# Performance work log

Measured on AMD Instinct MI355X. Metric: run time of the kernel, lower is better.

Reference implementation:

```python
import jax, jax.numpy as jnp
import numpy as np

DIM = 1024
B, S = 4, 2048

def setup_inputs() -> dict:
    key = jax.random.key(0)
    ks = jax.random.split(key, 4)
    x = jax.random.normal(ks[0], (B, S, DIM), dtype=jnp.float32)
    mask = jax.random.randint(ks[1], (B, S, S), 0, 2, dtype=jnp.int32)
    Wqkv = jax.random.normal(ks[2], (DIM, 3 * DIM), dtype=jnp.float32) / np.sqrt(DIM)
    bqkv = jnp.zeros((3 * DIM,), dtype=jnp.float32)
    Wout = jax.random.normal(ks[3], (DIM, DIM), dtype=jnp.float32) / np.sqrt(DIM)
    bout = jnp.zeros((DIM,), dtype=jnp.float32)
    return {"x": x, "mask": mask, "Wqkv": Wqkv, "bqkv": bqkv, "Wout": Wout, "bout": bout}

def reference(x, mask, Wqkv, bqkv, Wout, bout):
    dim = x.shape[-1]
    qkv = x @ Wqkv + bqkv                      # [B,S,3*dim]
    q, k, v = jnp.split(qkv, 3, axis=-1)       # each [B,S,dim]
    scores = jnp.einsum('bqd,bkd->bqk', q, k) / jnp.sqrt(jnp.float32(dim))
    # faithful to torch: masked positions set to 1e-10 (NOT -inf)
    scores = jnp.where(mask == 0, jnp.float32(1e-10), scores)
    attn = jax.nn.softmax(scores, axis=-1)     # dropout is identity in eval
    out = jnp.einsum('bqk,bkd->bqd', attn, v)  # [B,S,dim]
    return out @ Wout + bout
```

## Files before the change

### kernel.cpp

```cpp
#include <hip/hip_runtime.h>


typedef __attribute__((ext_vector_type(8))) short short8;
typedef __attribute__((ext_vector_type(4))) float f32x4;
typedef unsigned short u16;

#define SEQ 2048
#define NB 4

static __device__ __forceinline__ u16 f2bf(float f) {
    unsigned int u = __builtin_bit_cast(unsigned int, f);
    u += 0x7fffu + ((u >> 16) & 1u);
    return (u16)(u >> 16);
}
static __device__ __forceinline__ float bf2f(u16 h) {
    unsigned int u = ((unsigned int)h) << 16;
    return __builtin_bit_cast(float, u);
}

static __device__ __forceinline__ void gld16(const u16* l, const u16* g) {
    __builtin_amdgcn_global_load_lds(
        (__attribute__((address_space(1))) void*)(g),
        (__attribute__((address_space(3))) void*)(l),
        16, 0, 0);
}

__global__ __launch_bounds__(256) void cvt_bf16(const float* __restrict__ s,
                                                u16* __restrict__ d, long n) {
    long i = ((long)blockIdx.x * 256 + threadIdx.x) * 8;
    if (i >= n) return;
    f32x4 a = *(const f32x4*)(s + i);
    f32x4 b = *(const f32x4*)(s + i + 4);
    short8 o;
    o[0] = (short)f2bf(a.x); o[1] = (short)f2bf(a.y);
    o[2] = (short)f2bf(a.z); o[3] = (short)f2bf(a.w);
    o[4] = (short)f2bf(b.x); o[5] = (short)f2bf(b.y);
    o[6] = (short)f2bf(b.z); o[7] = (short)f2bf(b.w);
    *(short8*)(d + i) = o;
}

__global__ __launch_bounds__(256) void transpose_cvt(const float* __restrict__ in,
                                                     u16* __restrict__ out,
                                                     int R, int C) {
    __shared__ float t[32][33];
    const int c0 = blockIdx.x * 32;
    const int r0 = blockIdx.y * 32;
    const int x = threadIdx.x & 31;
    const int y = (threadIdx.x >> 5) * 4;
    #pragma unroll
    for (int i = 0; i < 4; i++)
        t[y + i][x] = in[(long)(r0 + y + i) * C + c0 + x];
    __syncthreads();
    #pragma unroll
    for (int i = 0; i < 4; i++)
        out[(long)(c0 + y + i) * R + r0 + x] = f2bf(t[x][y + i]);
}

__global__ __launch_bounds__(256) void transpose_v(const u16* __restrict__ qkv,
                                                   u16* __restrict__ vt) {
    __shared__ u16 t[32][33];
    const int b = blockIdx.z;
    const int s0 = blockIdx.y * 32;
    const int d0 = blockIdx.x * 32;
    const int x = threadIdx.x & 31;
    const int y = (threadIdx.x >> 5) * 4;
    const u16* src = qkv + (long)b * SEQ * 3072 + 2048;
    u16* dst = vt + (long)b * 1024 * SEQ;
    #pragma unroll
    for (int i = 0; i < 4; i++)
        t[y + i][x] = src[(long)(s0 + y + i) * 3072 + d0 + x];
    __syncthreads();
    #pragma unroll
    for (int i = 0; i < 4; i++)
        dst[(long)(d0 + y + i) * SEQ + s0 + x] = t[x][y + i];
}

template<int EPI>
__global__ __launch_bounds__(512) void gemm256d(
    const u16* __restrict__ Ap, long lda, long aBatch,
    const u16* __restrict__ Bp, long ldb, long bBatch,
    void* __restrict__ Cp, long ldc, long cBatch,
    const float* __restrict__ bias, float scale, int K, int nbx)
{
    __shared__ __attribute__((aligned(16))) u16 lds[2][4][8192];

    const int T = K >> 6;
    const int tid = threadIdx.x;
    const int lane = tid & 63;
    const int wave = tid >> 6;
    const int wm = wave >> 2;
    const int wn = wave & 3;
    const int m16 = lane & 15;
    const int quad = lane >> 4;
    const int b = blockIdx.z;

    const int nwg = gridDim.x;
    int wg = blockIdx.x;
    if ((nwg & 7) == 0)
        wg = (wg & 7) * (nwg >> 3) + (wg >> 3);
    const int bx = wg % nbx;
    const int by = wg / nbx;
    const long gm0 = (long)by * 256;
    const long gn0 = (long)bx * 256;

    const u16* A = Ap + (long)b * aBatch;
    const u16* B = Bp + (long)b * bBatch;

    const int rl = lane >> 3;
    const int lsl = ((lane & 7) ^ rl) * 8;
    const long aR = gm0 + wave * 8 + rl;
    const long bR = gn0 + (wave >> 2) * 64 + (wave & 3) * 8 + rl;

#define STGD(sl, tt) do { \
    const long kc_ = (long)(tt) << 6; \
    u16* l_ = &lds[sl][0][0]; \
    gld16(l_ + 0 * 8192 + wave * 512,       A + (aR)       * lda + kc_ + lsl); \
    gld16(l_ + 0 * 8192 + (8 + wave) * 512, A + (aR + 128) * lda + kc_ + lsl); \
    gld16(l_ + 1 * 8192 + wave * 512,       A + (aR + 64)  * lda + kc_ + lsl); \
    gld16(l_ + 1 * 8192 + (8 + wave) * 512, A + (aR + 192) * lda + kc_ + lsl); \
    gld16(l_ + 2 * 8192 + wave * 512,       B + (bR)       * ldb + kc_ + lsl); \
    gld16(l_ + 2 * 8192 + (8 + wave) * 512, B + (bR + 128) * ldb + kc_ + lsl); \
    gld16(l_ + 3 * 8192 + wave * 512,       B + (bR + 32)  * ldb + kc_ + lsl); \
    gld16(l_ + 3 * 8192 + (8 + wave) * 512, B + (bR + 160) * ldb + kc_ + lsl); \
} while (0)

    const int s0 = quad ^ (m16 & 7);
    const int aBase = (wm * 64 + m16) * 64;
    const int bBase = (wn * 32 + m16) * 64;
    const int aoff0 = aBase + s0 * 8, aoff1 = aBase + (s0 ^ 4) * 8;
    const int boff0 = bBase + s0 * 8, boff1 = bBase + (s0 ^ 4) * 8;

    short8 aF[4][2], b0F[2][2], b1F[2][2];
    f32x4 acc[8][4];
    #pragma unroll
    for (int mi = 0; mi < 8; mi++)
        #pragma unroll
        for (int ni = 0; ni < 4; ni++)
            acc[mi][ni] = (f32x4){0.f, 0.f, 0.f, 0.f};

#define TILE_COMPUTE(sl) do { \
    const u16* l = &lds[sl][0][0]; \
    _Pragma("unroll") \
    for (int mfl = 0; mfl < 4; ++mfl) { \
        aF[mfl][0] = *(const short8*)(l + aoff0 + mfl * 1024); \
        aF[mfl][1] = *(const short8*)(l + aoff1 + mfl * 1024); \
    } \
    _Pragma("unroll") \
    for (int nj = 0; nj < 2; ++nj) { \
        b0F[nj][0] = *(const short8*)(l + 2 * 8192 + boff0 + nj * 1024); \
        b0F[nj][1] = *(const short8*)(l + 2 * 8192 + boff1 + nj * 1024); \
        b1F[nj][0] = *(const short8*)(l + 3 * 8192 + boff0 + nj * 1024); \
        b1F[nj][1] = *(const short8*)(l + 3 * 8192 + boff1 + nj * 1024); \
    } \
    _Pragma("unroll") \
    for (int mi = 0; mi < 4; ++mi) \
        _Pragma("unroll") \
        for (int nj = 0; nj < 4; ++nj) { \
            const short8* bf = (nj < 2) ? &b0F[nj][0] : &b1F[nj - 2][0]; \
            acc[mi][nj] = __builtin_amdgcn_mfma_f32_16x16x32_bf16( \
                aF[mi][0], bf[0], acc[mi][nj], 0, 0, 0); \
            acc[mi][nj] = __builtin_amdgcn_mfma_f32_16x16x32_bf16( \
                aF[mi][1], bf[1], acc[mi][nj], 0, 0, 0); \
        } \
    _Pragma("unroll") \
    for (int mfl = 0; mfl < 4; ++mfl) { \
        aF[mfl][0] = *(const short8*)(l + 1 * 8192 + aoff0 + mfl * 1024); \
        aF[mfl][1] = *(const short8*)(l + 1 * 8192 + aoff1 + mfl * 1024); \
    } \
    _Pragma("unroll") \
    for (int mi = 0; mi < 4; ++mi) \
        _Pragma("unroll") \
        for (int nj = 0; nj < 4; ++nj) { \
            const short8* bf = (nj < 2) ? &b0F[nj][0] : &b1F[nj - 2][0]; \
            acc[4 + mi][nj] = __builtin_amdgcn_mfma_f32_16x16x32_bf16( \
                aF[mi][0], bf[0], acc[4 + mi][nj], 0, 0, 0); \
            acc[4 + mi][nj] = __builtin_amdgcn_mfma_f32_16x16x32_bf16( \
                aF[mi][1], bf[1], acc[4 + mi][nj], 0, 0, 0); \
        } \
} while (0)

    STGD(0, 0);
    __syncthreads();

    for (int t = 0; t < T; t += 2) {
        if (t + 1 < T) STGD(1, t + 1);
        TILE_COMPUTE(0);
        __syncthreads();
        if (t + 2 < T) STGD(0, t + 2);
        TILE_COMPUTE(1);
        __syncthreads();
    }

    const long row0 = gm0 + wm * 128 + quad * 4;
    const long colbase = gn0 + wn * 64 + m16;
    if (EPI == 0 || EPI == 1) {
        u16* C = (u16*)Cp + (long)b * cBatch;
        float bv[4];
        #pragma unroll
        for (int ni = 0; ni < 4; ++ni)
            bv[ni] = (EPI == 0 && bias)
                   ? bias[colbase + (ni >> 1) * 32 + (ni & 1) * 16] : 0.f;
        #pragma unroll
        for (int mi = 0; mi < 8; ++mi) {
            const long rb = row0 + (mi >> 2) * 64 + (mi & 3) * 16;
            #pragma unroll
            for (int r = 0; r < 4; ++r) {
                u16* Crow = C + (rb + r) * ldc + colbase;
                #pragma unroll
                for (int ni = 0; ni < 4; ++ni) {
                    const float vv = (EPI == 1) ? acc[mi][ni][r] * scale
                                                : acc[mi][ni][r] + bv[ni];
                    Crow[(ni >> 1) * 32 + (ni & 1) * 16] = f2bf(vv);
                }
            }
        }
    } else {
        float* C = (float*)Cp + (long)b * cBatch;
        float bv[4];
        #pragma unroll
        for (int ni = 0; ni < 4; ++ni)
            bv[ni] = bias ? bias[colbase + (ni >> 1) * 32 + (ni & 1) * 16] : 0.f;
        #pragma unroll
        for (int mi = 0; mi < 8; ++mi) {
            const long rb = row0 + (mi >> 2) * 64 + (mi & 3) * 16;
            #pragma unroll
            for (int r = 0; r < 4; ++r) {
                float* Crow = C + (rb + r) * ldc + colbase;
                #pragma unroll
                for (int ni = 0; ni < 4; ++ni)
                    Crow[(ni >> 1) * 32 + (ni & 1) * 16] = acc[mi][ni][r] + bv[ni];
            }
        }
    }
#undef STGD
#undef TILE_COMPUTE
}

template<int EPI>
__global__ __launch_bounds__(512) void gemm192(
    const u16* __restrict__ Ap, long lda, long aBatch,
    const u16* __restrict__ Bp, long ldb, long bBatch,
    void* __restrict__ Cp, long ldc, long cBatch,
    const float* __restrict__ bias, float scale, int K, int nbx)
{
    __shared__ __attribute__((aligned(16))) u16 lds[2][28672];

    const int T = K >> 6;
    const int tid = threadIdx.x;
    const int lane = tid & 63;
    const int wave = tid >> 6;
    const int wm = wave >> 2;
    const int wn = wave & 3;
    const int m16 = lane & 15;
    const int quad = lane >> 4;
    const int b = blockIdx.z;

    const int nwg = gridDim.x;
    int wg = blockIdx.x;
    if ((nwg & 7) == 0)
        wg = (wg & 7) * (nwg >> 3) + (wg >> 3);
    const int bx = wg % nbx;
    const int by = wg / nbx;
    const long gm0 = (long)by * 256;
    const long gn0 = (long)bx * 192;

    const u16* A = Ap + (long)b * aBatch;
    const u16* B = Bp + (long)b * bBatch;

    const int rl = lane >> 3;
    const int lsl = ((lane & 7) ^ rl) * 8;
    const long aR = gm0 + wave * 8 + rl;
    const long bR = gn0 + wave * 8 + rl;

#define STG192(sl, tt) do { \
    const long kc_ = (long)(tt) << 6; \
    u16* l_ = &lds[sl][0]; \
    gld16(l_ + wave * 512,              A + (aR)       * lda + kc_ + lsl); \
    gld16(l_ + (8 + wave) * 512,        A + (aR + 128) * lda + kc_ + lsl); \
    gld16(l_ + 8192 + wave * 512,       A + (aR + 64)  * lda + kc_ + lsl); \
    gld16(l_ + 8192 + (8 + wave) * 512, A + (aR + 192) * lda + kc_ + lsl); \
    gld16(l_ + 16384 + wave * 512,        B + (bR)       * ldb + kc_ + lsl); \
    gld16(l_ + 16384 + (8 + wave) * 512,  B + (bR + 64)  * ldb + kc_ + lsl); \
    gld16(l_ + 16384 + (16 + wave) * 512, B + (bR + 128) * ldb + kc_ + lsl); \
} while (0)

    const int s0 = quad ^ (m16 & 7);
    const int aBase = (wm * 64 + m16) * 64;
    const int bBase = (wn * 48 + m16) * 64;
    const int aoff0 = aBase + s0 * 8, aoff1 = aBase + (s0 ^ 4) * 8;
    const int boff0 = bBase + s0 * 8, boff1 = bBase + (s0 ^ 4) * 8;

    short8 aF[4][2], bF[3][2];
    f32x4 acc[8][3];
    #pragma unroll
    for (int mi = 0; mi < 8; mi++)
        #pragma unroll
        for (int ni = 0; ni < 3; ni++)
            acc[mi][ni] = (f32x4){0.f, 0.f, 0.f, 0.f};

#define TILE192(sl) do { \
    const u16* l = &lds[sl][0]; \
    _Pragma("unroll") \
    for (int mfl = 0; mfl < 4; ++mfl) { \
        aF[mfl][0] = *(const short8*)(l + aoff0 + mfl * 1024); \
        aF[mfl][1] = *(const short8*)(l + aoff1 + mfl * 1024); \
    } \
    _Pragma("unroll") \
    for (int nj = 0; nj < 3; ++nj) { \
        bF[nj][0] = *(const short8*)(l + 16384 + boff0 + nj * 1024); \
        bF[nj][1] = *(const short8*)(l + 16384 + boff1 + nj * 1024); \
    } \
    _Pragma("unroll") \
    for (int mi = 0; mi < 4; ++mi) \
        _Pragma("unroll") \
        for (int nj = 0; nj < 3; ++nj) { \
            acc[mi][nj] = __builtin_amdgcn_mfma_f32_16x16x32_bf16( \
                aF[mi][0], bF[nj][0], acc[mi][nj], 0, 0, 0); \
            acc[mi][nj] = __builtin_amdgcn_mfma_f32_16x16x32_bf16( \
                aF[mi][1], bF[nj][1], acc[mi][nj], 0, 0, 0); \
        } \
    _Pragma("unroll") \
    for (int mfl = 0; mfl < 4; ++mfl) { \
        aF[mfl][0] = *(const short8*)(l + 8192 + aoff0 + mfl * 1024); \
        aF[mfl][1] = *(const short8*)(l + 8192 + aoff1 + mfl * 1024); \
    } \
    _Pragma("unroll") \
    for (int mi = 0; mi < 4; ++mi) \
        _Pragma("unroll") \
        for (int nj = 0; nj < 3; ++nj) { \
            acc[4 + mi][nj] = __builtin_amdgcn_mfma_f32_16x16x32_bf16( \
                aF[mi][0], bF[nj][0], acc[4 + mi][nj], 0, 0, 0); \
            acc[4 + mi][nj] = __builtin_amdgcn_mfma_f32_16x16x32_bf16( \
                aF[mi][1], bF[nj][1], acc[4 + mi][nj], 0, 0, 0); \
        } \
} while (0)

    STG192(0, 0);
    __syncthreads();

    for (int t = 0; t < T; t += 2) {
        if (t + 1 < T) STG192(1, t + 1);
        TILE192(0);
        __syncthreads();
        if (t + 2 < T) STG192(0, t + 2);
        TILE192(1);
        __syncthreads();
    }

    const long row0 = gm0 + wm * 128 + quad * 4;
    const long colbase = gn0 + wn * 48 + m16;
    if (EPI == 0 || EPI == 1) {
        u16* C = (u16*)Cp + (long)b * cBatch;
        float bv[3];
        #pragma unroll
        for (int ni = 0; ni < 3; ++ni)
            bv[ni] = (EPI == 0 && bias) ? bias[colbase + ni * 16] : 0.f;
        #pragma unroll
        for (int mi = 0; mi < 8; ++mi) {
            const long rb = row0 + (mi >> 2) * 64 + (mi & 3) * 16;
            #pragma unroll
            for (int r = 0; r < 4; ++r) {
                u16* Crow = C + (rb + r) * ldc + colbase;
                #pragma unroll
                for (int ni = 0; ni < 3; ++ni) {
                    const float vv = (EPI == 1) ? acc[mi][ni][r] * scale
                                                : acc[mi][ni][r] + bv[ni];
                    Crow[ni * 16] = f2bf(vv);
                }
            }
        }
    } else {
        float* C = (float*)Cp + (long)b * cBatch;
        float bv[3];
        #pragma unroll
        for (int ni = 0; ni < 3; ++ni)
            bv[ni] = bias ? bias[colbase + ni * 16] : 0.f;
        #pragma unroll
        for (int mi = 0; mi < 8; ++mi) {
            const long rb = row0 + (mi >> 2) * 64 + (mi & 3) * 16;
            #pragma unroll
            for (int r = 0; r < 4; ++r) {
                float* Crow = C + (rb + r) * ldc + colbase;
                #pragma unroll
                for (int ni = 0; ni < 3; ++ni)
                    Crow[ni * 16] = acc[mi][ni][r] + bv[ni];
            }
        }
    }
#undef STG192
#undef TILE192
}

template<int EPI>
__global__ __launch_bounds__(256, 2) void gemm128d(
    const u16* __restrict__ Ap, long lda, long aBatch,
    const u16* __restrict__ Bp, long ldb, long bBatch,
    void* __restrict__ Cp, long ldc, long cBatch,
    const float* __restrict__ bias, float scale, int K, int nbx)
{
    __shared__ __attribute__((aligned(16))) u16 lds[2][2][8192];

    const int T = K >> 6;
    const int tid = threadIdx.x;
    const int lane = tid & 63;
    const int wave = tid >> 6;
    const int wm = wave >> 1;
    const int wn = wave & 1;
    const int m16 = lane & 15;
    const int quad = lane >> 4;
    const int b = blockIdx.z;

    const int nwg = gridDim.x;
    int wg = blockIdx.x;
    if ((nwg & 7) == 0)
        wg = (wg & 7) * (nwg >> 3) + (wg >> 3);
    const int bx = wg % nbx;
    const int by = wg / nbx;
    const long m0 = (long)by * 128;
    const long n0 = (long)bx * 128;

    const u16* A = Ap + (long)b * aBatch;
    const u16* B = Bp + (long)b * bBatch;

    const int rl = lane >> 3;
    const int lsl = ((lane & 7) ^ rl) * 8;
    const long aR = m0 + wave * 8 + rl;
    const long bR = n0 + wave * 8 + rl;

#define STG128(sl, tt) do { \
    const long kc_ = (long)(tt) << 6; \
    _Pragma("unroll") \
    for (int i_ = 0; i_ < 4; ++i_) { \
        gld16(&lds[sl][0][(i_ * 4 + wave) * 512], A + (aR + i_ * 32) * lda + kc_ + lsl); \
        gld16(&lds[sl][1][(i_ * 4 + wave) * 512], B + (bR + i_ * 32) * ldb + kc_ + lsl); \
    } \
} while (0)

    const int s0 = quad ^ (m16 & 7);
    const int aoff0 = (wm * 64 + m16) * 64 + s0 * 8;
    const int aoff1 = (wm * 64 + m16) * 64 + (s0 ^ 4) * 8;
    const int boff0 = (wn * 64 + m16) * 64 + s0 * 8;
    const int boff1 = (wn * 64 + m16) * 64 + (s0 ^ 4) * 8;

    short8 aF[4][2], bF[4][2];
    f32x4 acc[4][4];
    #pragma unroll
    for (int mi = 0; mi < 4; mi++)
        #pragma unroll
        for (int ni = 0; ni < 4; ni++)
            acc[mi][ni] = (f32x4){0.f, 0.f, 0.f, 0.f};

#define TILE128(sl) do { \
    const u16* la = &lds[sl][0][0]; \
    const u16* lb = &lds[sl][1][0]; \
    _Pragma("unroll") \
    for (int mf = 0; mf < 4; ++mf) { \
        aF[mf][0] = *(const short8*)(la + aoff0 + mf * 1024); \
        aF[mf][1] = *(const short8*)(la + aoff1 + mf * 1024); \
    } \
    _Pragma("unroll") \
    for (int nj = 0; nj < 4; ++nj) { \
        bF[nj][0] = *(const short8*)(lb + boff0 + nj * 1024); \
        bF[nj][1] = *(const short8*)(lb + boff1 + nj * 1024); \
    } \
    _Pragma("unroll") \
    for (int mi = 0; mi < 4; ++mi) \
        _Pragma("unroll") \
        for (int nj = 0; nj < 4; ++nj) { \
            acc[mi][nj] = __builtin_amdgcn_mfma_f32_16x16x32_bf16( \
                aF[mi][0], bF[nj][0], acc[mi][nj], 0, 0, 0); \
            acc[mi][nj] = __builtin_amdgcn_mfma_f32_16x16x32_bf16( \
                aF[mi][1], bF[nj][1], acc[mi][nj], 0, 0, 0); \
        } \
} while (0)

    STG128(0, 0);
    __syncthreads();

    for (int t = 0; t < T; t += 2) {
        if (t + 1 < T) STG128(1, t + 1);
        TILE128(0);
        __syncthreads();
        if (t + 2 < T) STG128(0, t + 2);
        TILE128(1);
        __syncthreads();
    }

    const long row0 = m0 + wm * 64 + quad * 4;
    const long colbase = n0 + wn * 64 + m16;
    if (EPI == 0 || EPI == 1) {
        u16* C = (u16*)Cp + (long)b * cBatch;
        float bv[4];
        #pragma unroll
        for (int ni = 0; ni < 4; ++ni)
            bv[ni] = (EPI == 0 && bias) ? bias[colbase + ni * 16] : 0.f;
        #pragma unroll
        for (int mi = 0; mi < 4; ++mi)
            #pragma unroll
            for (int r = 0; r < 4; ++r) {
                u16* Crow = C + (row0 + mi * 16 + r) * ldc + colbase;
                #pragma unroll
                for (int ni = 0; ni < 4; ++ni) {
                    const float vv = (EPI == 1) ? acc[mi][ni][r] * scale
                                                : acc[mi][ni][r] + bv[ni];
                    Crow[ni * 16] = f2bf(vv);
                }
            }
    } else {
        float* C = (float*)Cp + (long)b * cBatch;
        float bv[4];
        #pragma unroll
        for (int ni = 0; ni < 4; ++ni)
            bv[ni] = bias ? bias[colbase + ni * 16] : 0.f;
        #pragma unroll
        for (int mi = 0; mi < 4; ++mi)
            #pragma unroll
            for (int r = 0; r < 4; ++r) {
                float* Crow = C + (row0 + mi * 16 + r) * ldc + colbase;
                #pragma unroll
                for (int ni = 0; ni < 4; ++ni)
                    Crow[ni * 16] = acc[mi][ni][r] + bv[ni];
            }
    }
#undef STG128
#undef TILE128
}

__global__ __launch_bounds__(256) void softmax2048(u16* __restrict__ S,
                                                   const int* __restrict__ mask) {
    const long row = blockIdx.x;
    u16* p = S + row * SEQ;
    const int* mrow = mask + row * SEQ;
    const int tid = threadIdx.x;

    short8 v = *(const short8*)(p + tid * 8);
    uint4 mw0 = *(const uint4*)(mrow + tid * 8);
    uint4 mw1 = *(const uint4*)(mrow + tid * 8 + 4);
    const unsigned int* mwv = (const unsigned int*)&mw0;

    float f[8];
    #pragma unroll
    for (int j = 0; j < 8; j++) {
        const unsigned int mv = (j < 4) ? mwv[j] : ((const unsigned int*)&mw1)[j - 4];
        f[j] = (mv == 0u) ? 1e-10f : bf2f((u16)v[j]);
    }

    float m = f[0];
    #pragma unroll
    for (int j = 1; j < 8; j++) m = fmaxf(m, f[j]);
    #pragma unroll
    for (int i = 1; i < 64; i <<= 1) m = fmaxf(m, __shfl_xor(m, i));

    __shared__ float redm[4], reds[4];
    if ((tid & 63) == 0) redm[tid >> 6] = m;
    __syncthreads();
    m = fmaxf(fmaxf(redm[0], redm[1]), fmaxf(redm[2], redm[3]));

    float e[8], s = 0.f;
    #pragma unroll
    for (int j = 0; j < 8; j++) { e[j] = __expf(f[j] - m); s += e[j]; }
    #pragma unroll
    for (int i = 1; i < 64; i <<= 1) s += __shfl_xor(s, i);
    if ((tid & 63) == 0) reds[tid >> 6] = s;
    __syncthreads();
    s = reds[0] + reds[1] + reds[2] + reds[3];

    const float inv = 1.f / s;
    short8 o;
    #pragma unroll
    for (int j = 0; j < 8; j++) o[j] = (short)f2bf(e[j] * inv);
    *(short8*)(p + tid * 8) = o;
}

extern "C" void kernel_launch(void* const* d_in, const int* in_sizes, int n_in,
                              void* d_out, int out_size, void* d_ws, size_t ws_size,
                              hipStream_t stream) {
    const float* x    = (const float*)d_in[0];
    const int*   mask = (const int*)d_in[1];
    const float* Wqkv = (const float*)d_in[2];
    const float* bqkv = (const float*)d_in[3];
    const float* Wout = (const float*)d_in[4];
    const float* bout = (const float*)d_in[5];
    float* out = (float*)d_out;

    char* ws = (char*)d_ws;
    u16* xh   = (u16*)(ws + 0);
    u16* wqt  = (u16*)(ws + 16777216);
    u16* sc   = (u16*)(ws + 0);
    u16* wot  = (u16*)(ws + 33554432);
    u16* qkv  = (u16*)(ws + 35651584);
    u16* attn = (u16*)(ws + 35651584);
    u16* vt   = (u16*)(ws + 85983232);

    cvt_bf16<<<4096, 256, 0, stream>>>(x, xh, 8388608);
    transpose_cvt<<<dim3(96, 32), 256, 0, stream>>>(Wqkv, wqt, 1024, 3072);
    transpose_cvt<<<dim3(32, 32), 256, 0, stream>>>(Wout, wot, 1024, 1024);

    gemm192<0><<<dim3(512, 1, 1), 512, 0, stream>>>(
        xh, 1024, 0, wqt, 1024, 0, qkv, 3072, 0, bqkv, 1.f, 1024, 16);

    transpose_v<<<dim3(32, 64, NB), 256, 0, stream>>>(qkv, vt);

    gemm256d<1><<<dim3(64, 1, NB), 512, 0, stream>>>(
        qkv, 3072, (long)SEQ * 3072, qkv + 1024, 3072, (long)SEQ * 3072,
        sc, SEQ, (long)SEQ * SEQ, nullptr, 0.03125f, 1024, 8);

    softmax2048<<<dim3(NB * SEQ), 256, 0, stream>>>(sc, mask);

    gemm128d<0><<<dim3(128, 1, NB), 256, 0, stream>>>(
        sc, SEQ, (long)SEQ * SEQ, vt, SEQ, (long)1024 * SEQ,
        attn, 1024, (long)SEQ * 1024, nullptr, 1.f, 2048, 8);

    gemm128d<2><<<dim3(512, 1, 1), 256, 0, stream>>>(
        attn, 1024, 0, wot, 1024, 0, out, 1024, 0, bout, 1.f, 1024, 8);
}
```

Before: 199.4 us.

## Replace 128x128 GEMM with 256x128 tile, 8-wave kernel for PV and output projection

Replaces the 128x128, 4-wave GEMM used for attn@V and the output projection with a 256x128 tile, 512-thread kernel in which each wave computes a 128x32 sub-tile in two passes over the A halves. The larger M tile is meant to improve data reuse per LDS byte and cut global traffic for B. The cost is more LDS per block (48KB double-buffered), fewer workgroups (256 per GEMM), and possibly lower occupancy.

```diff
diff --git a/kernel.cpp b/kernel.cpp
--- a/kernel.cpp
+++ b/kernel.cpp
@@ -392,20 +392,20 @@
 }
 
 template<int EPI>
-__global__ __launch_bounds__(256, 2) void gemm128d(
+__global__ __launch_bounds__(512) void gemm256x128(
     const u16* __restrict__ Ap, long lda, long aBatch,
     const u16* __restrict__ Bp, long ldb, long bBatch,
     void* __restrict__ Cp, long ldc, long cBatch,
     const float* __restrict__ bias, float scale, int K, int nbx)
 {
-    __shared__ __attribute__((aligned(16))) u16 lds[2][2][8192];
+    __shared__ __attribute__((aligned(16))) u16 lds[2][3][8192];
 
     const int T = K >> 6;
     const int tid = threadIdx.x;
     const int lane = tid & 63;
     const int wave = tid >> 6;
-    const int wm = wave >> 1;
-    const int wn = wave & 1;
+    const int wm = wave >> 2;
+    const int wn = wave & 3;
     const int m16 = lane & 15;
     const int quad = lane >> 4;
     const int b = blockIdx.z;
@@ -416,114 +416,133 @@
         wg = (wg & 7) * (nwg >> 3) + (wg >> 3);
     const int bx = wg % nbx;
     const int by = wg / nbx;
-    const long m0 = (long)by * 128;
-    const long n0 = (long)bx * 128;
+    const long gm0 = (long)by * 256;
+    const long gn0 = (long)bx * 128;
 
     const u16* A = Ap + (long)b * aBatch;
     const u16* B = Bp + (long)b * bBatch;
 
     const int rl = lane >> 3;
     const int lsl = ((lane & 7) ^ rl) * 8;
-    const long aR = m0 + wave * 8 + rl;
-    const long bR = n0 + wave * 8 + rl;
-
-#define STG128(sl, tt) do { \
+    const long aR = gm0 + wave * 8 + rl;
+    const long bR = gn0 + wave * 8 + rl;
+
+#define STGX(sl, tt) do { \
     const long kc_ = (long)(tt) << 6; \
-    _Pragma("unroll") \
-    for (int i_ = 0; i_ < 4; ++i_) { \
-        gld16(&lds[sl][0][(i_ * 4 + wave) * 512], A + (aR + i_ * 32) * lda + kc_ + lsl); \
-        gld16(&lds[sl][1][(i_ * 4 + wave) * 512], B + (bR + i_ * 32) * ldb + kc_ + lsl); \
-    } \
+    u16* l_ = &lds[sl][0][0]; \
+    gld16(l_ + 0 * 8192 + wave * 512,       A + (aR)       * lda + kc_ + lsl); \
+    gld16(l_ + 0 * 8192 + (8 + wave) * 512, A + (aR + 128) * lda + kc_ + lsl); \
+    gld16(l_ + 1 * 8192 + wave * 512,       A + (aR + 64)  * lda + kc_ + lsl); \
+    gld16(l_ + 1 * 8192 + (8 + wave) * 512, A + (aR + 192) * lda + kc_ + lsl); \
+    gld16(l_ + 2 * 8192 + wave * 512,       B + (bR)       * ldb + kc_ + lsl); \
+    gld16(l_ + 2 * 8192 + (8 + wave) * 512, B + (bR + 64)  * ldb + kc_ + lsl); \
 } while (0)
 
     const int s0 = quad ^ (m16 & 7);
-    const int aoff0 = (wm * 64 + m16) * 64 + s0 * 8;
-    const int aoff1 = (wm * 64 + m16) * 64 + (s0 ^ 4) * 8;
-    const int boff0 = (wn * 64 + m16) * 64 + s0 * 8;
-    const int boff1 = (wn * 64 + m16) * 64 + (s0 ^ 4) * 8;
-
-    short8 aF[4][2], bF[4][2];
-    f32x4 acc[4][4];
-    #pragma unroll
-    for (int mi = 0; mi < 4; mi++)
-        #pragma unroll
-        for (int ni = 0; ni < 4; ni++)
+    const int aBase = (wm * 64 + m16) * 64;
+    const int bBase = (wn * 32 + m16) * 64;
+    const int aoff0 = aBase + s0 * 8, aoff1 = aBase + (s0 ^ 4) * 8;
+    const int boff0 = bBase + s0 * 8, boff1 = bBase + (s0 ^ 4) * 8;
+
+    short8 aF[4][2], bF[2][2];
+    f32x4 acc[8][2];
+    #pragma unroll
+    for (int mi = 0; mi < 8; mi++)
+        #pragma unroll
+        for (int ni = 0; ni < 2; ni++)
             acc[mi][ni] = (f32x4){0.f, 0.f, 0.f, 0.f};
 
-#define TILE128(sl) do { \
-    const u16* la = &lds[sl][0][0]; \
-    const u16* lb = &lds[sl][1][0]; \
-    _Pragma("unroll") \
-    for (int mf = 0; mf < 4; ++mf) { \
-        aF[mf][0] = *(const short8*)(la + aoff0 + mf * 1024); \
-        aF[mf][1] = *(const short8*)(la + aoff1 + mf * 1024); \
-    } \
-    _Pragma("unroll") \
-    for (int nj = 0; nj < 4; ++nj) { \
-        bF[nj][0] = *(const short8*)(lb + boff0 + nj * 1024); \
-        bF[nj][1] = *(const short8*)(lb + boff1 + nj * 1024); \
+#define TILEX(sl) do { \
+    const u16* l = &lds[sl][0][0]; \
+    _Pragma("unroll") \
+    for (int mfl = 0; mfl < 4; ++mfl) { \
+        aF[mfl][0] = *(const short8*)(l + aoff0 + mfl * 1024); \
+        aF[mfl][1] = *(const short8*)(l + aoff1 + mfl * 1024); \
+    } \
+    _Pragma("unroll") \
+    for (int nj = 0; nj < 2; ++nj) { \
+        bF[nj][0] = *(const short8*)(l + 2 * 8192 + boff0 + nj * 1024); \
+        bF[nj][1] = *(const short8*)(l + 2 * 8192 + boff1 + nj * 1024); \
     } \
     _Pragma("unroll") \
     for (int mi = 0; mi < 4; ++mi) \
         _Pragma("unroll") \
-        for (int nj = 0; nj < 4; ++nj) { \
+        for (int nj = 0; nj < 2; ++nj) { \
             acc[mi][nj] = __builtin_amdgcn_mfma_f32_16x16x32_bf16( \
                 aF[mi][0], bF[nj][0], acc[mi][nj], 0, 0, 0); \
             acc[mi][nj] = __builtin_amdgcn_mfma_f32_16x16x32_bf16( \
                 aF[mi][1], bF[nj][1], acc[mi][nj], 0, 0, 0); \
         } \
+    _Pragma("unroll") \
+    for (int mfl = 0; mfl < 4; ++mfl) { \
+        aF[mfl][0] = *(const short8*)(l + 1 * 8192 + aoff0 + mfl * 1024); \
+        aF[mfl][1] = *(const short8*)(l + 1 * 8192 + aoff1 + mfl * 1024); \
+    } \
+    _Pragma("unroll") \
+    for (int mi = 0; mi < 4; ++mi) \
+        _Pragma("unroll") \
+        for (int nj = 0; nj < 2; ++nj) { \
+            acc[4 + mi][nj] = __builtin_amdgcn_mfma_f32_16x16x32_bf16( \
+                aF[mi][0], bF[nj][0], acc[4 + mi][nj], 0, 0, 0); \
+            acc[4 + mi][nj] = __builtin_amdgcn_mfma_f32_16x16x32_bf16( \
+                aF[mi][1], bF[nj][1], acc[4 + mi][nj], 0, 0, 0); \
+        } \
 } while (0)
 
-    STG128(0, 0);
+    STGX(0, 0);
     __syncthreads();
 
     for (int t = 0; t < T; t += 2) {
-        if (t + 1 < T) STG128(1, t + 1);
-        TILE128(0);
+        if (t + 1 < T) STGX(1, t + 1);
+        TILEX(0);
         __syncthreads();
-        if (t + 2 < T) STG128(0, t + 2);
-        TILE128(1);
+        if (t + 2 < T) STGX(0, t + 2);
+        TILEX(1);
         __syncthreads();
     }
 
-    const long row0 = m0 + wm * 64 + quad * 4;
-    const long colbase = n0 + wn * 64 + m16;
+    const long row0 = gm0 + wm * 128 + quad * 4;
+    const long colbase = gn0 + wn * 32 + m16;
     if (EPI == 0 || EPI == 1) {
         u16* C = (u16*)Cp + (long)b * cBatch;
-        float bv[4];
-        #pragma unroll
-        for (int ni = 0; ni < 4; ++ni)
+        float bv[2];
+        #pragma unroll
+        for (int ni = 0; ni < 2; ++ni)
             bv[ni] = (EPI == 0 && bias) ? bias[colbase + ni * 16] : 0.f;
         #pragma unroll
-        for (int mi = 0; mi < 4; ++mi)
+        for (int mi = 0; mi < 8; ++mi) {
+            const long rb = row0 + (mi >> 2) * 64 + (mi & 3) * 16;
             #pragma unroll
             for (int r = 0; r < 4; ++r) {
-                u16* Crow = C + (row0 + mi * 16 + r) * ldc + colbase;
+                u16* Crow = C + (rb + r) * ldc + colbase;
                 #pragma unroll
-                for (int ni = 0; ni < 4; ++ni) {
+                for (int ni = 0; ni < 2; ++ni) {
                     const float vv = (EPI == 1) ? acc[mi][ni][r] * scale
                                                 : acc[mi][ni][r] + bv[ni];
                     Crow[ni * 16] = f2bf(vv);
                 }
             }
+        }
     } else {
         float* C = (float*)Cp + (long)b * cBatch;
-        float bv[4];
-        #pragma unroll
-        for (int ni = 0; ni < 4; ++ni)
+        float bv[2];
+        #pragma unroll
+        for (int ni = 0; ni < 2; ++ni)
             bv[ni] = bias ? bias[colbase + ni * 16] : 0.f;
         #pragma unroll
-        for (int mi = 0; mi < 4; ++mi)
+        for (int mi = 0; mi < 8; ++mi) {
+            const long rb = row0 + (mi >> 2) * 64 + (mi & 3) * 16;
             #pragma unroll
             for (int r = 0; r < 4; ++r) {
-                float* Crow = C + (row0 + mi * 16 + r) * ldc + colbase;
+                float* Crow = C + (rb + r) * ldc + colbase;
                 #pragma unroll
-                for (int ni = 0; ni < 4; ++ni)
+                for (int ni = 0; ni < 2; ++ni)
                     Crow[ni * 16] = acc[mi][ni][r] + bv[ni];
             }
+        }
     }
-#undef STG128
-#undef TILE128
+#undef STGX
+#undef TILEX
 }
 
 __global__ __launch_bounds__(256) void softmax2048(u16* __restrict__ S,
@@ -607,10 +626,10 @@
 
     softmax2048<<<dim3(NB * SEQ), 256, 0, stream>>>(sc, mask);
 
-    gemm128d<0><<<dim3(128, 1, NB), 256, 0, stream>>>(
+    gemm256x128<0><<<dim3(64, 1, NB), 512, 0, stream>>>(
         sc, SEQ, (long)SEQ * SEQ, vt, SEQ, (long)1024 * SEQ,
         attn, 1024, (long)SEQ * 1024, nullptr, 1.f, 2048, 8);
 
-    gemm128d<2><<<dim3(512, 1, 1), 256, 0, stream>>>(
+    gemm256x128<2><<<dim3(256, 1, 1), 512, 0, stream>>>(
         attn, 1024, 0, wot, 1024, 0, out, 1024, 0, bout, 1.f, 1024, 8);
 }
```

Result: no change. 200.5 us (+0.6%).

## Load QK^T B operand directly from global into registers, halving LDS staging

Applied to the files above, without the earlier changes.

In the 256x256 score GEMM, the B (key) tile is no longer staged through LDS. Each wave loads its own B fragments from global memory straight into registers, double-buffered one k-step ahead, while only A goes through LDS. This halves LDS footprint and LDS traffic, which may allow higher occupancy. In exchange, B data that was shared via LDS is now loaded redundantly by the two wave rows, with uncoalesced 16-byte row loads and more register pressure.

```diff
diff --git a/kernel.cpp b/kernel.cpp
--- a/kernel.cpp
+++ b/kernel.cpp
@@ -76,13 +76,13 @@
 }
 
 template<int EPI>
-__global__ __launch_bounds__(512) void gemm256d(
+__global__ __launch_bounds__(512) void gemm256b(
     const u16* __restrict__ Ap, long lda, long aBatch,
     const u16* __restrict__ Bp, long ldb, long bBatch,
     void* __restrict__ Cp, long ldc, long cBatch,
     const float* __restrict__ bias, float scale, int K, int nbx)
 {
-    __shared__ __attribute__((aligned(16))) u16 lds[2][4][8192];
+    __shared__ __attribute__((aligned(16))) u16 lds[2][2][8192];
 
     const int T = K >> 6;
     const int tid = threadIdx.x;
@@ -109,28 +109,33 @@
     const int rl = lane >> 3;
     const int lsl = ((lane & 7) ^ rl) * 8;
     const long aR = gm0 + wave * 8 + rl;
-    const long bR = gn0 + (wave >> 2) * 64 + (wave & 3) * 8 + rl;
-
-#define STGD(sl, tt) do { \
+
+#define STGA(sl, tt) do { \
     const long kc_ = (long)(tt) << 6; \
     u16* l_ = &lds[sl][0][0]; \
-    gld16(l_ + 0 * 8192 + wave * 512,       A + (aR)       * lda + kc_ + lsl); \
-    gld16(l_ + 0 * 8192 + (8 + wave) * 512, A + (aR + 128) * lda + kc_ + lsl); \
-    gld16(l_ + 1 * 8192 + wave * 512,       A + (aR + 64)  * lda + kc_ + lsl); \
-    gld16(l_ + 1 * 8192 + (8 + wave) * 512, A + (aR + 192) * lda + kc_ + lsl); \
-    gld16(l_ + 2 * 8192 + wave * 512,       B + (bR)       * ldb + kc_ + lsl); \
-    gld16(l_ + 2 * 8192 + (8 + wave) * 512, B + (bR + 128) * ldb + kc_ + lsl); \
-    gld16(l_ + 3 * 8192 + wave * 512,       B + (bR + 32)  * ldb + kc_ + lsl); \
-    gld16(l_ + 3 * 8192 + (8 + wave) * 512, B + (bR + 160) * ldb + kc_ + lsl); \
+    gld16(l_ + wave * 512,              A + (aR)       * lda + kc_ + lsl); \
+    gld16(l_ + (8 + wave) * 512,        A + (aR + 128) * lda + kc_ + lsl); \
+    gld16(l_ + 8192 + wave * 512,       A + (aR + 64)  * lda + kc_ + lsl); \
+    gld16(l_ + 8192 + (8 + wave) * 512, A + (aR + 192) * lda + kc_ + lsl); \
 } while (0)
 
     const int s0 = quad ^ (m16 & 7);
     const int aBase = (wm * 64 + m16) * 64;
-    const int bBase = (wn * 32 + m16) * 64;
     const int aoff0 = aBase + s0 * 8, aoff1 = aBase + (s0 ^ 4) * 8;
-    const int boff0 = bBase + s0 * 8, boff1 = bBase + (s0 ^ 4) * 8;
-
-    short8 aF[4][2], b0F[2][2], b1F[2][2];
+
+    const u16* Bw = B + (gn0 + wn * 64 + m16) * ldb + quad * 8;
+
+#define LDB(F, tt) do { \
+    const long kc_ = (long)(tt) << 6; \
+    _Pragma("unroll") \
+    for (int nj_ = 0; nj_ < 4; ++nj_) { \
+        const u16* p_ = Bw + (long)((nj_ >> 1) * 32 + (nj_ & 1) * 16) * ldb + kc_; \
+        F[nj_][0] = *(const short8*)(p_); \
+        F[nj_][1] = *(const short8*)(p_ + 32); \
+    } \
+} while (0)
+
+    short8 aF[4][2], bC[4][2], bN[4][2];
     f32x4 acc[8][4];
     #pragma unroll
     for (int mi = 0; mi < 8; mi++)
@@ -138,7 +143,7 @@
         for (int ni = 0; ni < 4; ni++)
             acc[mi][ni] = (f32x4){0.f, 0.f, 0.f, 0.f};
 
-#define TILE_COMPUTE(sl) do { \
+#define TILEB(sl, BF) do { \
     const u16* l = &lds[sl][0][0]; \
     _Pragma("unroll") \
     for (int mfl = 0; mfl < 4; ++mfl) { \
@@ -146,48 +151,42 @@
         aF[mfl][1] = *(const short8*)(l + aoff1 + mfl * 1024); \
     } \
     _Pragma("unroll") \
-    for (int nj = 0; nj < 2; ++nj) { \
-        b0F[nj][0] = *(const short8*)(l + 2 * 8192 + boff0 + nj * 1024); \
-        b0F[nj][1] = *(const short8*)(l + 2 * 8192 + boff1 + nj * 1024); \
-        b1F[nj][0] = *(const short8*)(l + 3 * 8192 + boff0 + nj * 1024); \
-        b1F[nj][1] = *(const short8*)(l + 3 * 8192 + boff1 + nj * 1024); \
-    } \
-    _Pragma("unroll") \
     for (int mi = 0; mi < 4; ++mi) \
         _Pragma("unroll") \
         for (int nj = 0; nj < 4; ++nj) { \
-            const short8* bf = (nj < 2) ? &b0F[nj][0] : &b1F[nj - 2][0]; \
             acc[mi][nj] = __builtin_amdgcn_mfma_f32_16x16x32_bf16( \
-                aF[mi][0], bf[0], acc[mi][nj], 0, 0, 0); \
+                aF[mi][0], BF[nj][0], acc[mi][nj], 0, 0, 0); \
             acc[mi][nj] = __builtin_amdgcn_mfma_f32_16x16x32_bf16( \
-                aF[mi][1], bf[1], acc[mi][nj], 0, 0, 0); \
+                aF[mi][1], BF[nj][1], acc[mi][nj], 0, 0, 0); \
         } \
     _Pragma("unroll") \
     for (int mfl = 0; mfl < 4; ++mfl) { \
-        aF[mfl][0] = *(const short8*)(l + 1 * 8192 + aoff0 + mfl * 1024); \
-        aF[mfl][1] = *(const short8*)(l + 1 * 8192 + aoff1 + mfl * 1024); \
+        aF[mfl][0] = *(const short8*)(l + 8192 + aoff0 + mfl * 1024); \
+        aF[mfl][1] = *(const short8*)(l + 8192 + aoff1 + mfl * 1024); \
     } \
     _Pragma("unroll") \
     for (int mi = 0; mi < 4; ++mi) \
         _Pragma("unroll") \
         for (int nj = 0; nj < 4; ++nj) { \
-            const short8* bf = (nj < 2) ? &b0F[nj][0] : &b1F[nj - 2][0]; \
             acc[4 + mi][nj] = __builtin_amdgcn_mfma_f32_16x16x32_bf16( \
-                aF[mi][0], bf[0], acc[4 + mi][nj], 0, 0, 0); \
+                aF[mi][0], BF[nj][0], acc[4 + mi][nj], 0, 0, 0); \
             acc[4 + mi][nj] = __builtin_amdgcn_mfma_f32_16x16x32_bf16( \
-                aF[mi][1], bf[1], acc[4 + mi][nj], 0, 0, 0); \
+                aF[mi][1], BF[nj][1], acc[4 + mi][nj], 0, 0, 0); \
         } \
 } while (0)
 
-    STGD(0, 0);
+    STGA(0, 0);
+    LDB(bC, 0);
     __syncthreads();
 
     for (int t = 0; t < T; t += 2) {
-        if (t + 1 < T) STGD(1, t + 1);
-        TILE_COMPUTE(0);
+        if (t + 1 < T) STGA(1, t + 1);
+        LDB(bN, (t + 1 < T) ? t + 1 : t);
+        TILEB(0, bC);
         __syncthreads();
-        if (t + 2 < T) STGD(0, t + 2);
-        TILE_COMPUTE(1);
+        if (t + 2 < T) STGA(0, t + 2);
+        LDB(bC, (t + 2 < T) ? t + 2 : t);
+        TILEB(1, bN);
         __syncthreads();
     }
 
@@ -232,8 +231,9 @@
             }
         }
     }
-#undef STGD
-#undef TILE_COMPUTE
+#undef STGA
+#undef LDB
+#undef TILEB
 }
 
 template<int EPI>
@@ -601,7 +601,7 @@
 
     transpose_v<<<dim3(32, 64, NB), 256, 0, stream>>>(qkv, vt);
 
-    gemm256d<1><<<dim3(64, 1, NB), 512, 0, stream>>>(
+    gemm256b<1><<<dim3(64, 1, NB), 512, 0, stream>>>(
         qkv, 3072, (long)SEQ * 3072, qkv + 1024, 3072, (long)SEQ * 3072,
         sc, SEQ, (long)SEQ * SEQ, nullptr, 0.03125f, 1024, 8);
 
```

Measured after the change: 218.6 us. 1.1x slower.
